# Kernel optimization log

Measured on AMD Instinct MI355X. Metric: run time of the kernel, lower is better.

## Reference

```python
import jax, jax.numpy as jnp
import numpy as np

# ---- Mamba2 config (matches init_kwargs) ----
D_MODEL = 256
D_STATE = 64
D_CONV = 4
EXPAND = 4
HEADDIM = 64
CHUNK = 64
D_INNER = EXPAND * D_MODEL          # 1024
NHEADS = D_INNER // HEADDIM         # 16
CONV_DIM = D_INNER + 2 * D_STATE    # 1152
D_IN_PROJ = 2 * D_INNER + 2 * D_STATE + NHEADS  # 2192
BATCH = 4
SEQLEN = 4096


def setup_inputs() -> dict:
    key = jax.random.key(0)
    ks = jax.random.split(key, 8)
    return {
        "u": jax.random.normal(ks[0], (BATCH, SEQLEN, D_MODEL), jnp.float32),
        "in_proj_w": jax.random.normal(ks[1], (D_IN_PROJ, D_MODEL), jnp.float32) * 0.02,
        "conv_w": jax.random.normal(ks[2], (CONV_DIM, 1, D_CONV), jnp.float32) * 0.2,
        "conv_b": jnp.zeros((CONV_DIM,), jnp.float32),
        "dt_bias": jax.random.normal(ks[3], (NHEADS,), jnp.float32) * 0.1,
        "A_log": jax.random.normal(ks[4], (NHEADS,), jnp.float32) * 0.1,
        "D": jax.random.normal(ks[5], (NHEADS,), jnp.float32) * 0.1,
        "norm_w": jnp.ones((D_INNER,), jnp.float32),
        "out_proj_w": jax.random.normal(ks[6], (D_MODEL, D_INNER), jnp.float32) * 0.02,
    }


def _segsum_exp(x):
    """exp(segsum(x)) for x: (..., T). Lower-triangular, zero above diagonal.
    segsum[i, j] = sum_{k=j+1..i} x[k] = cumsum[i] - cumsum[j] (for i >= j)."""
    T = x.shape[-1]
    cs = jnp.cumsum(x, axis=-1)
    seg = cs[..., :, None] - cs[..., None, :]
    mask = jnp.tril(jnp.ones((T, T), dtype=bool))
    return jnp.where(mask, jnp.exp(seg), 0.0)


def _ssd(x, A, B, C, chunk):
    """SSD chunked scan.
    x: (b, l, h, p)  A: (b, l, h)  B, C: (b, l, n) (shared across heads)."""
    b, l, h, p = x.shape
    c = l // chunk
    xc = x.reshape(b, c, chunk, h, p)
    Ac = A.reshape(b, c, chunk, h).transpose(0, 3, 1, 2)  # (b, h, c, l)
    Bc = B.reshape(b, c, chunk, -1)
    Cc = C.reshape(b, c, chunk, -1)

    A_cs = jnp.cumsum(Ac, axis=-1)                         # (b, h, c, l)
    L = _segsum_exp(Ac)                                    # (b, h, c, l, l)
    # Intra-chunk (diagonal block) output
    Y_diag = jnp.einsum('bcln,bcsn,bhcls,bcshp->bclhp', Cc, Bc, L, xc)

    # Per-chunk states
    decay_states = jnp.exp(A_cs[..., -1:] - A_cs)          # (b, h, c, l)
    states = jnp.einsum('bcln,bhcl,bclhp->bchpn', Bc, decay_states, xc)
    states = jnp.concatenate([jnp.zeros_like(states[:, :1]), states], axis=1)

    # Inter-chunk recurrence via segsum over chunk-level decays
    A_last = jnp.pad(A_cs[..., -1], ((0, 0), (0, 0), (1, 0)))  # (b, h, c+1)
    decay_chunk = _segsum_exp(A_last)                          # (b, h, c+1, c+1)
    new_states = jnp.einsum('bhzc,bchpn->bzhpn', decay_chunk, states)
    states_prev, final_state = new_states[:, :-1], new_states[:, -1]

    # State -> output (off-diagonal contribution)
    state_decay_out = jnp.exp(A_cs)                        # (b, h, c, l)
    Y_off = jnp.einsum('bcln,bchpn,bhcl->bclhp', Cc, states_prev, state_decay_out)

    Y = (Y_diag + Y_off).reshape(b, l, h, p)
    return Y, final_state


def _silu(x):
    return x * jax.nn.sigmoid(x)


def reference(u, in_proj_w, conv_w, conv_b, dt_bias, A_log, D, norm_w, out_proj_w):
    b, l, _ = u.shape
    A = -jnp.exp(A_log)                                    # (h,)

    zxbcdt = u @ in_proj_w.T                               # (b, l, D_IN_PROJ)
    z = zxbcdt[..., :D_INNER]
    xBC = zxbcdt[..., D_INNER:D_INNER + CONV_DIM]
    dt = jax.nn.softplus(zxbcdt[..., -NHEADS:] + dt_bias)  # (b, l, h)

    # Causal depthwise conv1d (kernel D_CONV, left padding)
    xp = jnp.pad(xBC, ((0, 0), (D_CONV - 1, 0), (0, 0)))
    conv = conv_b
    for w in range(D_CONV):
        conv = conv + xp[:, w:w + l, :] * conv_w[:, 0, w]
    xBC = _silu(conv)

    x = xBC[..., :D_INNER].reshape(b, l, NHEADS, HEADDIM)
    Bm = xBC[..., D_INNER:D_INNER + D_STATE]
    Cm = xBC[..., -D_STATE:]

    y, _final_state = _ssd(x * dt[..., None], A * dt, Bm, Cm, CHUNK)
    y = y + x * D[:, None]
    y = y.reshape(b, l, D_INNER)

    # Gated RMSNorm
    y = y * _silu(z)
    y = y * jax.lax.rsqrt(jnp.mean(y * y, axis=-1, keepdims=True) + 1e-5) * norm_w

    return y @ out_proj_w.T                                # (b, l, d_model)
```

## Files before the change

### kernel.cpp

```cpp
#include <hip/hip_runtime.h>
#include <math.h>

#define BATCH   4
#define SEQLEN  4096
#define DMODEL  256
#define DINNER  1024
#define NHEADS  16
#define HEADDIM 64
#define DSTATE  64
#define CONVDIM 1152
#define DPROJ   2192
#define NCHUNK  64
#define CHUNK   64
#define ROWS    (BATCH*SEQLEN)
#define NPAD1   2304
#define TS      72

typedef unsigned short u16;
using frag  = __attribute__((ext_vector_type(8))) short;
using f32x4 = __attribute__((ext_vector_type(4))) float;

static __device__ __forceinline__ float bf2f(u16 u) {
    return __uint_as_float(((unsigned int)u) << 16);
}
static __device__ __forceinline__ u16 f2bf(float f) {
    unsigned int x = __float_as_uint(f);
    x += 0x7fffu + ((x >> 16) & 1u);
    return (u16)(x >> 16);
}

__global__ __launch_bounds__(256) void cvt_bf16(const float* __restrict__ in,
                                                u16* __restrict__ out,
                                                int total4, int valid_rows, int colshift)
{
    const int i = blockIdx.x * 256 + threadIdx.x;
    if (i >= total4) return;
    const int e = i * 4;
    const int row = e >> colshift;
    ushort4 o;
    if (row < valid_rows) {
        float4 v = *(const float4*)(in + e);
        o.x = f2bf(v.x); o.y = f2bf(v.y); o.z = f2bf(v.z); o.w = f2bf(v.w);
    } else {
        o.x = 0; o.y = 0; o.z = 0; o.w = 0;
    }
    *(ushort4*)(out + e) = o;
}

template<int KTOT, bool C_BF>
__global__ __launch_bounds__(256) void gemm_mfma(const u16* __restrict__ A,
                                                 const u16* __restrict__ W,
                                                 void* __restrict__ Cp,
                                                 int N)
{
    __shared__ u16 pool[128*136];
    u16* As = pool;
    u16* Ws = pool + 128*64;

    const int m0 = blockIdx.y * 128;
    const int n0 = blockIdx.x * 128;
    const int tid = threadIdx.x;
    const int lane = tid & 63;
    const int w  = tid >> 6;
    const int wr = w >> 1, wc = w & 1;

    const int srow = tid >> 3;
    const int scol = (tid & 7) * 8;
    const int ssw  = scol ^ ((srow & 7) * 8);

    const int lrow = lane & 15;
    const int kgrp = lane >> 4;
    const int swz  = (lrow & 7) * 8;

    f32x4 acc[4][4] = {};

    uint4 ra[4], rw[4];
    #pragma unroll
    for (int it = 0; it < 4; ++it) {
        const int r = it*32 + srow;
        ra[it] = *(const uint4*)(A + (size_t)(m0 + r)*KTOT + scol);
        rw[it] = *(const uint4*)(W + (size_t)(n0 + r)*KTOT + scol);
    }

    for (int kt = 0; kt < KTOT; kt += 64) {
        __syncthreads();
        #pragma unroll
        for (int it = 0; it < 4; ++it) {
            const int r = it*32 + srow;
            *(uint4*)&As[r*64 + ssw] = ra[it];
            *(uint4*)&Ws[r*64 + ssw] = rw[it];
        }
        __syncthreads();
        if (kt + 64 < KTOT) {
            #pragma unroll
            for (int it = 0; it < 4; ++it) {
                const int r = it*32 + srow;
                ra[it] = *(const uint4*)(A + (size_t)(m0 + r)*KTOT + kt + 64 + scol);
                rw[it] = *(const uint4*)(W + (size_t)(n0 + r)*KTOT + kt + 64 + scol);
            }
        }
        #pragma unroll
        for (int ks = 0; ks < 2; ++ks) {
            const int kx = (ks*32 + kgrp*8) ^ swz;
            frag af[4], bf[4];
            #pragma unroll
            for (int i = 0; i < 4; ++i)
                af[i] = *(const frag*)&As[(wr*64 + i*16 + lrow)*64 + kx];
            #pragma unroll
            for (int j = 0; j < 4; ++j)
                bf[j] = *(const frag*)&Ws[(wc*64 + j*16 + lrow)*64 + kx];
            #pragma unroll
            for (int i = 0; i < 4; ++i)
                #pragma unroll
                for (int j = 0; j < 4; ++j)
                    acc[i][j] = __builtin_amdgcn_mfma_f32_16x16x32_bf16(af[i], bf[j], acc[i][j], 0, 0, 0);
        }
    }

    if constexpr (C_BF) {
        __syncthreads();
        #pragma unroll
        for (int i = 0; i < 4; ++i)
            #pragma unroll
            for (int j = 0; j < 4; ++j)
                #pragma unroll
                for (int r = 0; r < 4; ++r)
                    pool[(wr*64 + i*16 + kgrp*4 + r)*136 + wc*64 + j*16 + lrow] =
                        f2bf(acc[i][j][r]);
        __syncthreads();
        #pragma unroll
        for (int q = 0; q < 8; ++q) {
            const int f  = q*2048 + tid*8;
            const int rl = f >> 7;
            const int cl = f & 127;
            const int col = n0 + cl;
            if (col < N)
                *(uint4*)((u16*)Cp + (size_t)(m0 + rl)*N + col) =
                    *(const uint4*)&pool[rl*136 + cl];
        }
    } else {
        #pragma unroll
        for (int i = 0; i < 4; ++i) {
            #pragma unroll
            for (int j = 0; j < 4; ++j) {
                const int col = n0 + wc*64 + j*16 + lrow;
                if (col < N) {
                    #pragma unroll
                    for (int r = 0; r < 4; ++r) {
                        const int row = m0 + wr*64 + i*16 + kgrp*4 + r;
                        ((float*)Cp)[(size_t)row * N + col] = acc[i][j][r];
                    }
                }
            }
        }
    }
}

__global__ __launch_bounds__(256) void conv_kernel(const u16* __restrict__ zxbcdt,
                                                   const float* __restrict__ conv_w,
                                                   const float* __restrict__ conv_b,
                                                   u16* __restrict__ xconv)
{
    const int idx = blockIdx.x * 256 + threadIdx.x;
    const int ch  = idx % CONVDIM;
    const int row = idx / CONVDIM;
    const int l   = row & (SEQLEN-1);
    const int b   = row >> 12;

    float acc = conv_b[ch];
    #pragma unroll
    for (int w = 0; w < 4; ++w) {
        const int ls = l - 3 + w;
        if (ls >= 0) {
            acc += bf2f(zxbcdt[(size_t)(b*SEQLEN + ls) * DPROJ + DINNER + ch]) * conv_w[ch*4 + w];
        }
    }
    xconv[idx] = f2bf(acc / (1.f + __expf(-acc)));
}

__global__ __launch_bounds__(256) void dt_kernel(const u16* __restrict__ zxbcdt,
                                                 const float* __restrict__ dt_bias,
                                                 const float* __restrict__ A_log,
                                                 float* __restrict__ dt,
                                                 float* __restrict__ dA)
{
    const int idx = blockIdx.x * 256 + threadIdx.x;
    const int h = idx & (NHEADS-1);
    const int row = idx >> 4;
    const float x = bf2f(zxbcdt[(size_t)row * DPROJ + (DPROJ - NHEADS) + h]) + dt_bias[h];
    const float sp = (x > 20.f) ? x : log1pf(__expf(x));
    dt[idx] = sp;
    dA[idx] = -__expf(A_log[h]) * sp;
}

__global__ __launch_bounds__(256) void ssd_phaseA(const u16* __restrict__ xconv,
                                                  const float* __restrict__ dtb,
                                                  const float* __restrict__ dAb,
                                                  u16* __restrict__ ybuf,
                                                  u16* __restrict__ statesT,
                                                  float* __restrict__ acs_g,
                                                  float* __restrict__ asum_g)
{
    const int h = blockIdx.x, c = blockIdx.y, b = blockIdx.z;
    const int tid = threadIdx.x;
    const int lane = tid & 63;
    const int w = tid >> 6;
    const int l0 = c * CHUNK;

    __shared__ u16 CtM[64*TS];
    __shared__ u16 Bt [64*TS];
    __shared__ u16 BtT[64*TS];
    __shared__ u16 xdtT[64*TS];
    __shared__ float a_cs[64];

    if (w == 0) {
        float v = dAb[(size_t)(b*SEQLEN + l0 + lane)*NHEADS + h];
        #pragma unroll
        for (int o = 1; o < 64; o <<= 1) {
            float t = __shfl_up(v, o, 64);
            if (lane >= o) v += t;
        }
        a_cs[lane] = v;
    }
    __syncthreads();
    const float a_last = a_cs[63];

    {
        const int j  = tid >> 2;
        const int q0 = (tid & 3) * 16;
        const u16* rp = xconv + (size_t)(b*SEQLEN + l0 + j) * CONVDIM;
        const float dtv = dtb[(size_t)(b*SEQLEN + l0 + j)*NHEADS + h];
        const float dec = __expf(a_last - a_cs[j]);

        *(uint4*)&CtM[j*TS + q0]     = *(const uint4*)(rp + DINNER + DSTATE + q0);
        *(uint4*)&CtM[j*TS + q0 + 8] = *(const uint4*)(rp + DINNER + DSTATE + q0 + 8);

        uint4 b0 = *(const uint4*)(rp + DINNER + q0);
        uint4 b1 = *(const uint4*)(rp + DINNER + q0 + 8);
        *(uint4*)&Bt[j*TS + q0]     = b0;
        *(uint4*)&Bt[j*TS + q0 + 8] = b1;
        unsigned int bw[8] = {b0.x, b0.y, b0.z, b0.w, b1.x, b1.y, b1.z, b1.w};
        #pragma unroll
        for (int s = 0; s < 8; ++s) {
            const int n0 = q0 + 2*s, n1 = n0 + 1;
            BtT[n0*TS + (j ^ (n0 & 0x38))] = f2bf(bf2f((u16)(bw[s] & 0xffff)) * dec);
            BtT[n1*TS + (j ^ (n1 & 0x38))] = f2bf(bf2f((u16)(bw[s] >> 16))    * dec);
        }

        uint4 x0 = *(const uint4*)(rp + h*HEADDIM + q0);
        uint4 x1 = *(const uint4*)(rp + h*HEADDIM + q0 + 8);
        unsigned int xw[8] = {x0.x, x0.y, x0.z, x0.w, x1.x, x1.y, x1.z, x1.w};
        #pragma unroll
        for (int s = 0; s < 8; ++s) {
            const int p0 = q0 + 2*s, p1 = p0 + 1;
            xdtT[p0*TS + (j ^ (p0 & 0x38))] = f2bf(bf2f((u16)(xw[s] & 0xffff)) * dtv);
            xdtT[p1*TS + (j ^ (p1 & 0x38))] = f2bf(bf2f((u16)(xw[s] >> 16))    * dtv);
        }
    }
    __syncthreads();

    const int lrow = lane & 15;
    const int kgrp = lane >> 4;

    f32x4 accG[4] = {};
    #pragma unroll
    for (int ks = 0; ks < 2; ++ks) {
        frag a = *(const frag*)&CtM[(w*16 + lrow)*TS + ks*32 + kgrp*8];
        #pragma unroll
        for (int cf = 0; cf < 4; ++cf) {
            frag bb = *(const frag*)&Bt[(cf*16 + lrow)*TS + ks*32 + kgrp*8];
            accG[cf] = __builtin_amdgcn_mfma_f32_16x16x32_bf16(a, bb, accG[cf], 0, 0, 0);
        }
    }

    {
        float aj[4];
        #pragma unroll
        for (int cf = 0; cf < 4; ++cf) aj[cf] = a_cs[cf*16 + lrow];
        #pragma unroll
        for (int r = 0; r < 4; ++r) {
            const int i = w*16 + kgrp*4 + r;
            const float ai = a_cs[i];
            #pragma unroll
            for (int cf = 0; cf < 4; ++cf) {
                const int jcol = cf*16 + lrow;
                const float g = (jcol <= i) ? accG[cf][r] * __expf(ai - aj[cf]) : 0.f;
                CtM[i*TS + jcol] = f2bf(g);
            }
        }
    }

    f32x4 accY[4] = {};
    #pragma unroll
    for (int ks = 0; ks < 2; ++ks) {
        frag a = *(const frag*)&CtM[(w*16 + lrow)*TS + ks*32 + kgrp*8];
        #pragma unroll
        for (int cf = 0; cf < 4; ++cf) {
            const int p = cf*16 + lrow;
            frag bb = *(const frag*)&xdtT[p*TS + ((ks*32 + kgrp*8) ^ (p & 0x38))];
            accY[cf] = __builtin_amdgcn_mfma_f32_16x16x32_bf16(a, bb, accY[cf], 0, 0, 0);
        }
    }
    #pragma unroll
    for (int r = 0; r < 4; ++r) {
        const int i = w*16 + kgrp*4 + r;
        u16* yp = ybuf + (size_t)(b*SEQLEN + l0 + i)*DINNER + h*HEADDIM;
        #pragma unroll
        for (int cf = 0; cf < 4; ++cf)
            yp[cf*16 + lrow] = f2bf(accY[cf][r]);
    }

    f32x4 accS[4] = {};
    #pragma unroll
    for (int ks = 0; ks < 2; ++ks) {
        const int pr = w*16 + lrow;
        frag a = *(const frag*)&xdtT[pr*TS + ((ks*32 + kgrp*8) ^ (pr & 0x38))];
        #pragma unroll
        for (int cf = 0; cf < 4; ++cf) {
            const int n = cf*16 + lrow;
            frag bb = *(const frag*)&BtT[n*TS + ((ks*32 + kgrp*8) ^ (n & 0x38))];
            accS[cf] = __builtin_amdgcn_mfma_f32_16x16x32_bf16(a, bb, accS[cf], 0, 0, 0);
        }
    }
    {
        u16* sp = statesT + (((size_t)b*NCHUNK + c)*NHEADS + h)*4096;
        #pragma unroll
        for (int r = 0; r < 4; ++r) {
            const int p = w*16 + kgrp*4 + r;
            #pragma unroll
            for (int cf = 0; cf < 4; ++cf)
                sp[p*64 + cf*16 + lrow] = f2bf(accS[cf][r]);
        }
    }

    if (tid < 64) acs_g[(((size_t)b*NCHUNK + c)*NHEADS + h)*CHUNK + tid] = a_cs[tid];
    if (tid == 0) asum_g[((size_t)b*NHEADS + h)*NCHUNK + c] = a_last;
}

__global__ __launch_bounds__(256) void ssd_scan(u16* __restrict__ statesT,
                                                const float* __restrict__ asum_g)
{
    const int gid = blockIdx.x;
    const int s = gid & 15;
    const int h = (gid >> 4) & (NHEADS-1);
    const int b = gid >> 8;
    const int elem = s*256 + threadIdx.x;

    const float* as = asum_g + ((size_t)b*NHEADS + h)*NCHUNK;
    float P = 0.f;
    for (int c = 0; c < NCHUNK; ++c) {
        const size_t idx = (((size_t)b*NCHUNK + c)*NHEADS + h)*4096 + elem;
        const float sv = bf2f(statesT[idx]);
        statesT[idx] = f2bf(P);
        P = P * __expf(as[c]) + sv;
    }
}

__global__ __launch_bounds__(256) void ssd_phaseC(const u16* __restrict__ xconv,
                                                  const u16* __restrict__ zxbcdt,
                                                  const u16* __restrict__ statesT,
                                                  const float* __restrict__ acs_g,
                                                  const float* __restrict__ Dvec,
                                                  u16* __restrict__ ybuf)
{
    const int h = blockIdx.x, c = blockIdx.y, b = blockIdx.z;
    const int tid = threadIdx.x;
    const int lane = tid & 63;
    const int w = tid >> 6;
    const int l0 = c * CHUNK;

    __shared__ u16 Ct [64*TS];
    __shared__ u16 SpT[64*TS];
    __shared__ float a_cs[64];

    if (tid < 64) a_cs[tid] = acs_g[(((size_t)b*NCHUNK + c)*NHEADS + h)*CHUNK + tid];
    {
        const int r  = tid >> 2;
        const int q0 = (tid & 3) * 16;
        const u16* cp = xconv + (size_t)(b*SEQLEN + l0 + r)*CONVDIM + DINNER + DSTATE;
        *(uint4*)&Ct[r*TS + q0]     = *(const uint4*)(cp + q0);
        *(uint4*)&Ct[r*TS + q0 + 8] = *(const uint4*)(cp + q0 + 8);
        const u16* spg = statesT + (((size_t)b*NCHUNK + c)*NHEADS + h)*4096 + r*64;
        *(uint4*)&SpT[r*TS + q0]     = *(const uint4*)(spg + q0);
        *(uint4*)&SpT[r*TS + q0 + 8] = *(const uint4*)(spg + q0 + 8);
    }
    __syncthreads();

    const int lrow = lane & 15;
    const int kgrp = lane >> 4;

    f32x4 acc[4] = {};
    #pragma unroll
    for (int ks = 0; ks < 2; ++ks) {
        frag a = *(const frag*)&Ct[(w*16 + lrow)*TS + ks*32 + kgrp*8];
        #pragma unroll
        for (int cf = 0; cf < 4; ++cf) {
            frag bb = *(const frag*)&SpT[(cf*16 + lrow)*TS + ks*32 + kgrp*8];
            acc[cf] = __builtin_amdgcn_mfma_f32_16x16x32_bf16(a, bb, acc[cf], 0, 0, 0);
        }
    }

    const float Dh = Dvec[h];
    #pragma unroll
    for (int r = 0; r < 4; ++r) {
        const int i = w*16 + kgrp*4 + r;
        const int l = l0 + i;
        const float e = __expf(a_cs[i]);
        const u16* xr = xconv  + (size_t)(b*SEQLEN + l)*CONVDIM + h*HEADDIM;
        const u16* zr = zxbcdt + (size_t)(b*SEQLEN + l)*DPROJ   + h*HEADDIM;
        u16* yp = ybuf + (size_t)(b*SEQLEN + l)*DINNER + h*HEADDIM;
        #pragma unroll
        for (int cf = 0; cf < 4; ++cf) {
            const int p = cf*16 + lrow;
            const float yv = bf2f(yp[p]) + e*acc[cf][r] + bf2f(xr[p])*Dh;
            const float zv = bf2f(zr[p]);
            yp[p] = f2bf(yv * (zv / (1.f + __expf(-zv))));
        }
    }
}

__global__ __launch_bounds__(256) void rmsnorm_kernel(u16* __restrict__ y,
                                                      const float* __restrict__ w)
{
    __shared__ float red[4];
    const int row = blockIdx.x;
    const int tid = threadIdx.x;
    ushort4* yp = (ushort4*)(y + (size_t)row * DINNER);
    ushort4 v = yp[tid];
    float f0 = bf2f(v.x), f1 = bf2f(v.y), f2 = bf2f(v.z), f3 = bf2f(v.w);
    float ss = f0*f0 + f1*f1 + f2*f2 + f3*f3;
    #pragma unroll
    for (int o = 32; o > 0; o >>= 1) ss += __shfl_down(ss, o);
    if ((tid & 63) == 0) red[tid >> 6] = ss;
    __syncthreads();
    const float total = red[0] + red[1] + red[2] + red[3];
    const float scale = rsqrtf(total * (1.f/1024.f) + 1e-5f);
    const float4 wv = ((const float4*)w)[tid];
    ushort4 o;
    o.x = f2bf(f0 * scale * wv.x);
    o.y = f2bf(f1 * scale * wv.y);
    o.z = f2bf(f2 * scale * wv.z);
    o.w = f2bf(f3 * scale * wv.w);
    yp[tid] = o;
}

extern "C" void kernel_launch(void* const* d_in, const int* in_sizes, int n_in,
                              void* d_out, int out_size, void* d_ws, size_t ws_size,
                              hipStream_t stream)
{
    const float* u          = (const float*)d_in[0];
    const float* in_proj_w  = (const float*)d_in[1];
    const float* conv_w     = (const float*)d_in[2];
    const float* conv_b     = (const float*)d_in[3];
    const float* dt_bias    = (const float*)d_in[4];
    const float* A_log      = (const float*)d_in[5];
    const float* Dvec       = (const float*)d_in[6];
    const float* norm_w     = (const float*)d_in[7];
    const float* out_proj_w = (const float*)d_in[8];
    float* out = (float*)d_out;

    float* dtb  = (float*)d_ws;
    float* dAb  = dtb  + (size_t)ROWS*NHEADS;
    float* acs  = dAb  + (size_t)ROWS*NHEADS;
    float* asum = acs  + (size_t)BATCH*NCHUNK*NHEADS*CHUNK;
    u16* zxbcdt = (u16*)(asum + (size_t)BATCH*NHEADS*NCHUNK);
    u16* xconv  = zxbcdt + (size_t)ROWS*DPROJ;
    u16* ybuf   = xconv  + (size_t)ROWS*CONVDIM;
    u16* states = ybuf   + (size_t)ROWS*DINNER;
    u16* w2b    = states + (size_t)BATCH*NCHUNK*NHEADS*DSTATE*HEADDIM;
    u16* u_bf   = states;
    u16* w1b    = states + (size_t)ROWS*DMODEL;

    cvt_bf16<<<(ROWS*DMODEL/4+255)/256, 256, 0, stream>>>(u, u_bf, ROWS*DMODEL/4, ROWS, 8);
    cvt_bf16<<<(NPAD1*DMODEL/4+255)/256, 256, 0, stream>>>(in_proj_w, w1b, NPAD1*DMODEL/4, DPROJ, 8);
    cvt_bf16<<<(DMODEL*DINNER/4+255)/256, 256, 0, stream>>>(out_proj_w, w2b, DMODEL*DINNER/4, DMODEL, 10);

    gemm_mfma<DMODEL, true><<<dim3(NPAD1/128, ROWS/128), 256, 0, stream>>>(u_bf, w1b, zxbcdt, DPROJ);

    conv_kernel<<<(ROWS*CONVDIM)/256, 256, 0, stream>>>(zxbcdt, conv_w, conv_b, xconv);
    dt_kernel<<<(ROWS*NHEADS)/256, 256, 0, stream>>>(zxbcdt, dt_bias, A_log, dtb, dAb);
    ssd_phaseA<<<dim3(NHEADS, NCHUNK, BATCH), 256, 0, stream>>>(xconv, dtb, dAb, ybuf, states, acs, asum);
    ssd_scan<<<BATCH*NHEADS*16, 256, 0, stream>>>(states, asum);
    ssd_phaseC<<<dim3(NHEADS, NCHUNK, BATCH), 256, 0, stream>>>(xconv, zxbcdt, states, acs, Dvec, ybuf);
    rmsnorm_kernel<<<ROWS, 256, 0, stream>>>(ybuf, norm_w);

    gemm_mfma<DINNER, false><<<dim3(DMODEL/128, ROWS/128), 256, 0, stream>>>(ybuf, w2b, out, DMODEL);
}
```

Before: 420.7 us.

## Fuse dt into SSD phase A, RMSNorm into out-proj GEMM, add nontemporal stores

Computes softplus(dt) and dA inline in ssd_phaseA, which removes the separate dt kernel and its buffers. Phase C now accumulates per-row sum of squares with atomics, and the output GEMM applies the RMSNorm scale and weight while staging A tiles into shared memory. This removes the standalone rmsnorm pass over ybuf. Phase A stages y and states through LDS for coalesced 16-byte nontemporal stores, and other writes also become nontemporal. The costs are an extra memset, per-element float atomics, extra conversion work in the GEMM load path, and a second bf16 rounding of the normalized input.

```diff
diff --git a/kernel.cpp b/kernel.cpp
--- a/kernel.cpp
+++ b/kernel.cpp
@@ -19,6 +19,7 @@
 typedef unsigned short u16;
 using frag  = __attribute__((ext_vector_type(8))) short;
 using f32x4 = __attribute__((ext_vector_type(4))) float;
+using u32x4 = __attribute__((ext_vector_type(4))) unsigned int;
 
 static __device__ __forceinline__ float bf2f(u16 u) {
     return __uint_as_float(((unsigned int)u) << 16);
@@ -27,6 +28,10 @@
     unsigned int x = __float_as_uint(f);
     x += 0x7fffu + ((x >> 16) & 1u);
     return (u16)(x >> 16);
+}
+static __device__ __forceinline__ void nt_store16(void* p, uint4 v) {
+    u32x4 t = {v.x, v.y, v.z, v.w};
+    __builtin_nontemporal_store(t, (u32x4*)p);
 }
 
 __global__ __launch_bounds__(256) void cvt_bf16(const float* __restrict__ in,
@@ -47,11 +52,13 @@
     *(ushort4*)(out + e) = o;
 }
 
-template<int KTOT, bool C_BF>
+template<int KTOT, bool C_BF, bool SCALE_A>
 __global__ __launch_bounds__(256) void gemm_mfma(const u16* __restrict__ A,
                                                  const u16* __restrict__ W,
                                                  void* __restrict__ Cp,
-                                                 int N)
+                                                 int N,
+                                                 const float* __restrict__ normv,
+                                                 const float* __restrict__ nw)
 {
     __shared__ u16 pool[128*136];
     u16* As = pool;
@@ -72,6 +79,13 @@
     const int kgrp = lane >> 4;
     const int swz  = (lrow & 7) * 8;
 
+    float ascale[4];
+    if constexpr (SCALE_A) {
+        #pragma unroll
+        for (int it = 0; it < 4; ++it)
+            ascale[it] = rsqrtf(normv[m0 + it*32 + srow] * (1.f/1024.f) + 1e-5f);
+    }
+
     f32x4 acc[4][4] = {};
 
     uint4 ra[4], rw[4];
@@ -87,7 +101,20 @@
         #pragma unroll
         for (int it = 0; it < 4; ++it) {
             const int r = it*32 + srow;
-            *(uint4*)&As[r*64 + ssw] = ra[it];
+            if constexpr (SCALE_A) {
+                uint4 v = ra[it];
+                unsigned int* pw = (unsigned int*)&v;
+                const float* nwp = nw + kt + scol;
+                #pragma unroll
+                for (int q = 0; q < 4; ++q) {
+                    const float lo = bf2f((u16)(pw[q] & 0xffff)) * ascale[it] * nwp[2*q];
+                    const float hi = bf2f((u16)(pw[q] >> 16))    * ascale[it] * nwp[2*q+1];
+                    pw[q] = (unsigned int)f2bf(lo) | ((unsigned int)f2bf(hi) << 16);
+                }
+                *(uint4*)&As[r*64 + ssw] = v;
+            } else {
+                *(uint4*)&As[r*64 + ssw] = ra[it];
+            }
             *(uint4*)&Ws[r*64 + ssw] = rw[it];
         }
         __syncthreads();
@@ -135,8 +162,8 @@
             const int cl = f & 127;
             const int col = n0 + cl;
             if (col < N)
-                *(uint4*)((u16*)Cp + (size_t)(m0 + rl)*N + col) =
-                    *(const uint4*)&pool[rl*136 + cl];
+                nt_store16((u16*)Cp + (size_t)(m0 + rl)*N + col,
+                           *(const uint4*)&pool[rl*136 + cl]);
         }
     } else {
         #pragma unroll
@@ -148,7 +175,8 @@
                     #pragma unroll
                     for (int r = 0; r < 4; ++r) {
                         const int row = m0 + wr*64 + i*16 + kgrp*4 + r;
-                        ((float*)Cp)[(size_t)row * N + col] = acc[i][j][r];
+                        __builtin_nontemporal_store(acc[i][j][r],
+                            (float*)Cp + (size_t)row * N + col);
                     }
                 }
             }
@@ -175,27 +203,13 @@
             acc += bf2f(zxbcdt[(size_t)(b*SEQLEN + ls) * DPROJ + DINNER + ch]) * conv_w[ch*4 + w];
         }
     }
-    xconv[idx] = f2bf(acc / (1.f + __expf(-acc)));
-}
-
-__global__ __launch_bounds__(256) void dt_kernel(const u16* __restrict__ zxbcdt,
-                                                 const float* __restrict__ dt_bias,
-                                                 const float* __restrict__ A_log,
-                                                 float* __restrict__ dt,
-                                                 float* __restrict__ dA)
-{
-    const int idx = blockIdx.x * 256 + threadIdx.x;
-    const int h = idx & (NHEADS-1);
-    const int row = idx >> 4;
-    const float x = bf2f(zxbcdt[(size_t)row * DPROJ + (DPROJ - NHEADS) + h]) + dt_bias[h];
-    const float sp = (x > 20.f) ? x : log1pf(__expf(x));
-    dt[idx] = sp;
-    dA[idx] = -__expf(A_log[h]) * sp;
+    __builtin_nontemporal_store(f2bf(acc / (1.f + __expf(-acc))), xconv + idx);
 }
 
 __global__ __launch_bounds__(256) void ssd_phaseA(const u16* __restrict__ xconv,
-                                                  const float* __restrict__ dtb,
-                                                  const float* __restrict__ dAb,
+                                                  const u16* __restrict__ zxbcdt,
+                                                  const float* __restrict__ dt_bias,
+                                                  const float* __restrict__ A_log,
                                                   u16* __restrict__ ybuf,
                                                   u16* __restrict__ statesT,
                                                   float* __restrict__ acs_g,
@@ -212,9 +226,14 @@
     __shared__ u16 BtT[64*TS];
     __shared__ u16 xdtT[64*TS];
     __shared__ float a_cs[64];
+    __shared__ float a_dt[64];
 
     if (w == 0) {
-        float v = dAb[(size_t)(b*SEQLEN + l0 + lane)*NHEADS + h];
+        const float raw = bf2f(zxbcdt[(size_t)(b*SEQLEN + l0 + lane)*DPROJ + (DPROJ - NHEADS) + h])
+                        + dt_bias[h];
+        const float sp = (raw > 20.f) ? raw : log1pf(__expf(raw));
+        a_dt[lane] = sp;
+        float v = -__expf(A_log[h]) * sp;
         #pragma unroll
         for (int o = 1; o < 64; o <<= 1) {
             float t = __shfl_up(v, o, 64);
@@ -229,7 +248,7 @@
         const int j  = tid >> 2;
         const int q0 = (tid & 3) * 16;
         const u16* rp = xconv + (size_t)(b*SEQLEN + l0 + j) * CONVDIM;
-        const float dtv = dtb[(size_t)(b*SEQLEN + l0 + j)*NHEADS + h];
+        const float dtv = a_dt[j];
         const float dec = __expf(a_last - a_cs[j]);
 
         *(uint4*)&CtM[j*TS + q0]     = *(const uint4*)(rp + DINNER + DSTATE + q0);
@@ -304,10 +323,9 @@
     #pragma unroll
     for (int r = 0; r < 4; ++r) {
         const int i = w*16 + kgrp*4 + r;
-        u16* yp = ybuf + (size_t)(b*SEQLEN + l0 + i)*DINNER + h*HEADDIM;
         #pragma unroll
         for (int cf = 0; cf < 4; ++cf)
-            yp[cf*16 + lrow] = f2bf(accY[cf][r]);
+            CtM[i*TS + cf*16 + lrow] = f2bf(accY[cf][r]);
     }
 
     f32x4 accS[4] = {};
@@ -322,15 +340,25 @@
             accS[cf] = __builtin_amdgcn_mfma_f32_16x16x32_bf16(a, bb, accS[cf], 0, 0, 0);
         }
     }
+    __syncthreads();
+    #pragma unroll
+    for (int r = 0; r < 4; ++r) {
+        const int p = w*16 + kgrp*4 + r;
+        #pragma unroll
+        for (int cf = 0; cf < 4; ++cf)
+            xdtT[p*TS + cf*16 + lrow] = f2bf(accS[cf][r]);
+    }
+    __syncthreads();
+
     {
-        u16* sp = statesT + (((size_t)b*NCHUNK + c)*NHEADS + h)*4096;
-        #pragma unroll
-        for (int r = 0; r < 4; ++r) {
-            const int p = w*16 + kgrp*4 + r;
-            #pragma unroll
-            for (int cf = 0; cf < 4; ++cf)
-                sp[p*64 + cf*16 + lrow] = f2bf(accS[cf][r]);
-        }
+        const int rr = tid >> 2;
+        const int q  = (tid & 3) * 16;
+        u16* yg = ybuf + (size_t)(b*SEQLEN + l0 + rr)*DINNER + h*HEADDIM + q;
+        nt_store16(yg,     *(const uint4*)&CtM[rr*TS + q]);
+        nt_store16(yg + 8, *(const uint4*)&CtM[rr*TS + q + 8]);
+        u16* sg = statesT + (((size_t)b*NCHUNK + c)*NHEADS + h)*4096 + tid*16;
+        nt_store16(sg,     *(const uint4*)&xdtT[rr*TS + q]);
+        nt_store16(sg + 8, *(const uint4*)&xdtT[rr*TS + q + 8]);
     }
 
     if (tid < 64) acs_g[(((size_t)b*NCHUNK + c)*NHEADS + h)*CHUNK + tid] = a_cs[tid];
@@ -361,7 +389,8 @@
                                                   const u16* __restrict__ statesT,
                                                   const float* __restrict__ acs_g,
                                                   const float* __restrict__ Dvec,
-                                                  u16* __restrict__ ybuf)
+                                                  u16* __restrict__ ybuf,
+                                                  float* __restrict__ normbuf)
 {
     const int h = blockIdx.x, c = blockIdx.y, b = blockIdx.z;
     const int tid = threadIdx.x;
@@ -409,39 +438,20 @@
         const u16* xr = xconv  + (size_t)(b*SEQLEN + l)*CONVDIM + h*HEADDIM;
         const u16* zr = zxbcdt + (size_t)(b*SEQLEN + l)*DPROJ   + h*HEADDIM;
         u16* yp = ybuf + (size_t)(b*SEQLEN + l)*DINNER + h*HEADDIM;
+        float ssq = 0.f;
         #pragma unroll
         for (int cf = 0; cf < 4; ++cf) {
             const int p = cf*16 + lrow;
             const float yv = bf2f(yp[p]) + e*acc[cf][r] + bf2f(xr[p])*Dh;
             const float zv = bf2f(zr[p]);
-            yp[p] = f2bf(yv * (zv / (1.f + __expf(-zv))));
-        }
-    }
-}
-
-__global__ __launch_bounds__(256) void rmsnorm_kernel(u16* __restrict__ y,
-                                                      const float* __restrict__ w)
-{
-    __shared__ float red[4];
-    const int row = blockIdx.x;
-    const int tid = threadIdx.x;
-    ushort4* yp = (ushort4*)(y + (size_t)row * DINNER);
-    ushort4 v = yp[tid];
-    float f0 = bf2f(v.x), f1 = bf2f(v.y), f2 = bf2f(v.z), f3 = bf2f(v.w);
-    float ss = f0*f0 + f1*f1 + f2*f2 + f3*f3;
-    #pragma unroll
-    for (int o = 32; o > 0; o >>= 1) ss += __shfl_down(ss, o);
-    if ((tid & 63) == 0) red[tid >> 6] = ss;
-    __syncthreads();
-    const float total = red[0] + red[1] + red[2] + red[3];
-    const float scale = rsqrtf(total * (1.f/1024.f) + 1e-5f);
-    const float4 wv = ((const float4*)w)[tid];
-    ushort4 o;
-    o.x = f2bf(f0 * scale * wv.x);
-    o.y = f2bf(f1 * scale * wv.y);
-    o.z = f2bf(f2 * scale * wv.z);
-    o.w = f2bf(f3 * scale * wv.w);
-    yp[tid] = o;
+            const float fin = yv * (zv / (1.f + __expf(-zv)));
+            ssq += fin * fin;
+            yp[p] = f2bf(fin);
+        }
+        #pragma unroll
+        for (int o = 1; o < 16; o <<= 1) ssq += __shfl_xor(ssq, o, 16);
+        if (lrow == 0) atomicAdd(normbuf + (size_t)(b*SEQLEN + l), ssq);
+    }
 }
 
 extern "C" void kernel_launch(void* const* d_in, const int* in_sizes, int n_in,
@@ -459,11 +469,10 @@
     const float* out_proj_w = (const float*)d_in[8];
     float* out = (float*)d_out;
 
-    float* dtb  = (float*)d_ws;
-    float* dAb  = dtb  + (size_t)ROWS*NHEADS;
-    float* acs  = dAb  + (size_t)ROWS*NHEADS;
-    float* asum = acs  + (size_t)BATCH*NCHUNK*NHEADS*CHUNK;
-    u16* zxbcdt = (u16*)(asum + (size_t)BATCH*NHEADS*NCHUNK);
+    float* acs     = (float*)d_ws;
+    float* asum    = acs  + (size_t)BATCH*NCHUNK*NHEADS*CHUNK;
+    float* normbuf = asum + (size_t)BATCH*NHEADS*NCHUNK;
+    u16* zxbcdt = (u16*)(normbuf + (size_t)ROWS);
     u16* xconv  = zxbcdt + (size_t)ROWS*DPROJ;
     u16* ybuf   = xconv  + (size_t)ROWS*CONVDIM;
     u16* states = ybuf   + (size_t)ROWS*DINNER;
@@ -471,18 +480,22 @@
     u16* u_bf   = states;
     u16* w1b    = states + (size_t)ROWS*DMODEL;
 
+    hipMemsetAsync(normbuf, 0, ROWS*sizeof(float), stream);
+
     cvt_bf16<<<(ROWS*DMODEL/4+255)/256, 256, 0, stream>>>(u, u_bf, ROWS*DMODEL/4, ROWS, 8);
     cvt_bf16<<<(NPAD1*DMODEL/4+255)/256, 256, 0, stream>>>(in_proj_w, w1b, NPAD1*DMODEL/4, DPROJ, 8);
     cvt_bf16<<<(DMODEL*DINNER/4+255)/256, 256, 0, stream>>>(out_proj_w, w2b, DMODEL*DINNER/4, DMODEL, 10);
 
-    gemm_mfma<DMODEL, true><<<dim3(NPAD1/128, ROWS/128), 256, 0, stream>>>(u_bf, w1b, zxbcdt, DPROJ);
+    gemm_mfma<DMODEL, true, false><<<dim3(NPAD1/128, ROWS/128), 256, 0, stream>>>(
+        u_bf, w1b, zxbcdt, DPROJ, nullptr, nullptr);
 
     conv_kernel<<<(ROWS*CONVDIM)/256, 256, 0, stream>>>(zxbcdt, conv_w, conv_b, xconv);
-    dt_kernel<<<(ROWS*NHEADS)/256, 256, 0, stream>>>(zxbcdt, dt_bias, A_log, dtb, dAb);
-    ssd_phaseA<<<dim3(NHEADS, NCHUNK, BATCH), 256, 0, stream>>>(xconv, dtb, dAb, ybuf, states, acs, asum);
+    ssd_phaseA<<<dim3(NHEADS, NCHUNK, BATCH), 256, 0, stream>>>(
+        xconv, zxbcdt, dt_bias, A_log, ybuf, states, acs, asum);
     ssd_scan<<<BATCH*NHEADS*16, 256, 0, stream>>>(states, asum);
-    ssd_phaseC<<<dim3(NHEADS, NCHUNK, BATCH), 256, 0, stream>>>(xconv, zxbcdt, states, acs, Dvec, ybuf);
-    rmsnorm_kernel<<<ROWS, 256, 0, stream>>>(ybuf, norm_w);
-
-    gemm_mfma<DINNER, false><<<dim3(DMODEL/128, ROWS/128), 256, 0, stream>>>(ybuf, w2b, out, DMODEL);
-}
+    ssd_phaseC<<<dim3(NHEADS, NCHUNK, BATCH), 256, 0, stream>>>(
+        xconv, zxbcdt, states, acs, Dvec, ybuf, normbuf);
+
+    gemm_mfma<DINNER, false, true><<<dim3(DMODEL/128, ROWS/128), 256, 0, stream>>>(
+        ybuf, w2b, out, DMODEL, normbuf, norm_w);
+}
```

After: 424.2 us. About the same (+0.8%).
